# Performance work log

Hardware: AMD Instinct MI355X
Metric: run time of the kernel (lower is better)

## Reference

```python
import jax, jax.numpy as jnp
import numpy as np

NUM_HEADS = 16
HEAD_DIM = 128


def rotate_half(x):
    x1, x2 = jnp.split(x, 2, axis=-1)
    return jnp.concatenate((-x2, x1), axis=-1)


def setup_inputs() -> dict:
    key = jax.random.key(0)
    ks = jax.random.split(key, 6)
    B, S, H = 2, 2048, 2048
    hidden_states = jax.random.normal(ks[0], (B, S, H), dtype=jnp.float32)
    # RoPE cos/sin tables (HF-style: half-dim freqs duplicated)
    inv_freq = 1.0 / (10000.0 ** (jnp.arange(0, HEAD_DIM, 2, dtype=jnp.float32) / HEAD_DIM))
    t = jnp.arange(S, dtype=jnp.float32)
    freqs = jnp.outer(t, inv_freq)                      # [S, HEAD_DIM/2]
    emb = jnp.concatenate((freqs, freqs), axis=-1)      # [S, HEAD_DIM]
    cos = jnp.cos(emb)
    sin = jnp.sin(emb)
    attention_mask = jnp.zeros((1, 1, S, S), dtype=jnp.float32)
    scale = 0.02
    Wq = jax.random.normal(ks[1], (H, H), dtype=jnp.float32) * scale
    Wk = jax.random.normal(ks[2], (H, H), dtype=jnp.float32) * scale
    Wv = jax.random.normal(ks[3], (H, H), dtype=jnp.float32) * scale
    Wo = jax.random.normal(ks[4], (H, H), dtype=jnp.float32) * scale
    return {"hidden_states": hidden_states, "cos": cos, "sin": sin,
            "attention_mask": attention_mask, "Wq": Wq, "Wk": Wk, "Wv": Wv, "Wo": Wo}


def reference(hidden_states, cos, sin, attention_mask, Wq, Wk, Wv, Wo):
    B, S, H = hidden_states.shape
    nh, hd = NUM_HEADS, HEAD_DIM
    # nn.Linear(bias=False): x @ W.T
    q = hidden_states @ Wq.T
    k = hidden_states @ Wk.T
    v = hidden_states @ Wv.T
    # [B, nh, S, hd]
    q = q.reshape(B, S, nh, hd).transpose(0, 2, 1, 3)
    k = k.reshape(B, S, nh, hd).transpose(0, 2, 1, 3)
    v = v.reshape(B, S, nh, hd).transpose(0, 2, 1, 3)
    # RoPE
    c = cos[None, None, :, :]
    s = sin[None, None, :, :]
    q = q * c + rotate_half(q) * s
    k = k * c + rotate_half(k) * s
    scores = jnp.einsum("bhqd,bhkd->bhqk", q, k) / jnp.sqrt(jnp.float32(hd))
    scores = scores + attention_mask
    attn = jax.nn.softmax(scores, axis=-1)
    out = jnp.einsum("bhqk,bhkd->bhqd", attn, v)
    out = out.transpose(0, 2, 1, 3).reshape(B, S, H)
    return out @ Wo.T
```

## Files before the change

### kernel.cpp

```cpp
#include <hip/hip_runtime.h>
#include <stdint.h>

typedef __bf16 bf16;
typedef __attribute__((ext_vector_type(4))) __bf16 bf16x4;
typedef __attribute__((ext_vector_type(8))) __bf16 bf16x8;
typedef __attribute__((ext_vector_type(4))) float f32x4;
typedef __attribute__((ext_vector_type(4))) short short4v;

__device__ __forceinline__ void gl2lds16(const void* g, void* l) {
  __builtin_amdgcn_global_load_lds(
      (__attribute__((address_space(1))) void*)(uintptr_t)g,
      (__attribute__((address_space(3))) void*)(uint32_t)(uintptr_t)l,
      16, 0, 0);
}

__device__ __forceinline__ f32x4 mfma_16x16x16(bf16x4 a, bf16x4 b, f32x4 c) {
#if defined(__HIP_DEVICE_COMPILE__)
  return __builtin_amdgcn_mfma_f32_16x16x16bf16_1k(
      __builtin_bit_cast(short4v, a), __builtin_bit_cast(short4v, b), c, 0, 0, 0);
#else
  return c;
#endif
}

__global__ __launch_bounds__(256) void cast_to_bf16(const float* __restrict__ x,
                                                    bf16* __restrict__ y, int n4) {
  int i = blockIdx.x * 256 + threadIdx.x;
  if (i >= n4) return;
  float4 v = ((const float4*)x)[i];
  bf16x4 o;
  o[0] = (bf16)v.x; o[1] = (bf16)v.y; o[2] = (bf16)v.z; o[3] = (bf16)v.w;
  ((bf16x4*)y)[i] = o;
}

__global__ __launch_bounds__(256) void cast_w4(const float* __restrict__ s0,
                                               const float* __restrict__ s1,
                                               const float* __restrict__ s2,
                                               const float* __restrict__ s3,
                                               bf16* __restrict__ d0, bf16* __restrict__ d1,
                                               bf16* __restrict__ d2, bf16* __restrict__ d3) {
  int i = blockIdx.x * 256 + threadIdx.x;
  int wsel = i >> 20;
  int j = i & 1048575;
  const float* s = wsel == 0 ? s0 : wsel == 1 ? s1 : wsel == 2 ? s2 : s3;
  bf16* d = wsel == 0 ? d0 : wsel == 1 ? d1 : wsel == 2 ? d2 : d3;
  float4 v = ((const float4*)s)[j];
  bf16x4 o;
  o[0] = (bf16)v.x; o[1] = (bf16)v.y; o[2] = (bf16)v.z; o[3] = (bf16)v.w;
  ((bf16x4*)d)[j] = o;
}

template <typename OutT>
__global__ __launch_bounds__(512) void gemm256(const bf16* __restrict__ A,
                                               const bf16* __restrict__ B,
                                               OutT* __restrict__ C,
                                               int M, int N, int K) {
  __shared__ bf16 As[2][2][128 * 64];
  __shared__ bf16 Bs[2][2][128 * 64];
  const int t = threadIdx.x;
  const int w = t >> 6;
  const int lane = t & 63;
  const int quad = lane >> 4;
  const int m16 = lane & 15;
  const int wr = w >> 2;
  const int wc = w & 3;
  const size_t rowA0 = (size_t)blockIdx.y * 256;
  const size_t rowB0 = (size_t)blockIdx.x * 256;

  f32x4 acc[8][4];
#pragma unroll
  for (int i = 0; i < 8; ++i)
#pragma unroll
    for (int j = 0; j < 4; ++j) { f32x4 z = {0.f, 0.f, 0.f, 0.f}; acc[i][j] = z; }

  const int srow = lane >> 3;
  const int sg = (lane & 7) ^ (srow & 7);

  auto stage = [&](int buf, int kt) {
#pragma unroll
    for (int h = 0; h < 2; ++h)
#pragma unroll
      for (int i = 0; i < 2; ++i) {
        const int ch = w * 2 + i;
        const int r = h * 128 + ch * 8 + srow;
        gl2lds16(A + (rowA0 + r) * (size_t)K + kt * 64 + sg * 8, &As[buf][h][ch * 512]);
        gl2lds16(B + (rowB0 + r) * (size_t)K + kt * 64 + sg * 8, &Bs[buf][h][ch * 512]);
      }
  };

  stage(0, 0);
  asm volatile("s_waitcnt vmcnt(0)" ::: "memory");
  __builtin_amdgcn_s_barrier();

  const int NT = K >> 6;
#pragma unroll 1
  for (int kt = 0; kt < NT; ++kt) {
    const int c = kt & 1;
    if (kt + 1 < NT) stage(c ^ 1, kt + 1);

#pragma unroll
    for (int p = 0; p < 4; ++p) {
      const int mh = p >> 1;
      const int nh = p & 1;
      bf16x8 af[4][2], bfr[2][2];
#pragma unroll
      for (int fm = 0; fm < 4; ++fm)
#pragma unroll
        for (int ks = 0; ks < 2; ++ks) {
          const int r = (mh * 4 + fm) * 16 + m16;
          af[fm][ks] = *(const bf16x8*)&As[c][wr][r * 64 + (((ks * 4 + quad) ^ (m16 & 7)) * 8)];
        }
#pragma unroll
      for (int fn = 0; fn < 2; ++fn)
#pragma unroll
        for (int ks = 0; ks < 2; ++ks) {
          const int r = (wc & 1) * 64 + (nh * 2 + fn) * 16 + m16;
          bfr[fn][ks] = *(const bf16x8*)&Bs[c][wc >> 1][r * 64 + (((ks * 4 + quad) ^ (m16 & 7)) * 8)];
        }
      __builtin_amdgcn_s_setprio(1);
#pragma unroll
      for (int fm = 0; fm < 4; ++fm)
#pragma unroll
        for (int fn = 0; fn < 2; ++fn)
#pragma unroll
          for (int ks = 0; ks < 2; ++ks)
            acc[mh * 4 + fm][nh * 2 + fn] = __builtin_amdgcn_mfma_f32_16x16x32_bf16(
                af[fm][ks], bfr[fn][ks], acc[mh * 4 + fm][nh * 2 + fn], 0, 0, 0);
      __builtin_amdgcn_s_setprio(0);
      if (p < 3) __builtin_amdgcn_s_barrier();
    }
    asm volatile("s_waitcnt vmcnt(0)" ::: "memory");
    __builtin_amdgcn_s_barrier();
  }

#pragma unroll
  for (int fm = 0; fm < 8; ++fm)
#pragma unroll
    for (int fn = 0; fn < 4; ++fn)
#pragma unroll
      for (int r = 0; r < 4; ++r) {
        size_t row = rowA0 + wr * 128 + fm * 16 + quad * 4 + r;
        size_t col = rowB0 + wc * 64 + fn * 16 + m16;
        float v = acc[fm][fn][r];
        if constexpr (__is_same(OutT, float)) C[row * N + col] = v;
        else                                  C[row * N + col] = (bf16)v;
      }
}

__global__ __launch_bounds__(256) void rope_kernel(bf16* __restrict__ X,
                                                   const float* __restrict__ cosp,
                                                   const float* __restrict__ sinp) {
  int tid = blockIdx.x * 256 + threadIdx.x;
  int d = tid & 63;
  int hh = (tid >> 6) & 31;
  int tok = tid >> 11;
  if (tok >= 4096) return;
  int s = tok & 2047;
  const float sl2e = 0.088388347648318447f * 1.4426950408889634f;
  float qs = hh < 16 ? sl2e : 1.0f;
  size_t base = (size_t)tok * 4096 + hh * 128 + d;
  float c = cosp[s * 128 + d];
  float sn = sinp[s * 128 + d];
  float x1 = (float)X[base];
  float x2 = (float)X[base + 64];
  X[base]      = (bf16)((x1 * c - x2 * sn) * qs);
  X[base + 64] = (bf16)((x2 * c + x1 * sn) * qs);
}

__global__ __launch_bounds__(256) void flash_attn(const bf16* __restrict__ Qg,
                                                  const bf16* __restrict__ Kg,
                                                  const bf16* __restrict__ Vt,
                                                  bf16* __restrict__ O) {
  __shared__ bf16 Ks[2][64 * 128];
  __shared__ bf16 Vs[2][128 * 64];

  const int t = threadIdx.x;
  const int w = t >> 6;
  const int lane = t & 63;
  const int quad = lane >> 4;
  const int m16 = lane & 15;
  const int qt = blockIdx.x;
  const int bh = blockIdx.y;
  const int b = bh >> 4;
  const int h = bh & 15;

  bf16x8 qf[2][4];
#pragma unroll
  for (int half = 0; half < 2; ++half) {
    const int qrow = qt * 128 + w * 32 + half * 16 + m16;
    const bf16* qp = Qg + (size_t)(b * 2048 + qrow) * 4096 + h * 128 + quad * 8;
#pragma unroll
    for (int ks = 0; ks < 4; ++ks) qf[half][ks] = *(const bf16x8*)(qp + ks * 32);
  }

  const int krl = lane >> 4;
  const int vrl = lane >> 3;
  const int vg = (lane & 7) ^ (vrl & 7);

  auto stage = [&](int buf, int kt) {
#pragma unroll
    for (int i = 0; i < 4; ++i) {
      const int c = w * 4 + i;
      const int krow = c * 4 + krl;
      const int kgg = (lane & 15) ^ (krow & 15);
      gl2lds16(Kg + (size_t)(b * 2048 + kt * 64 + krow) * 4096 + h * 128 + kgg * 8,
               &Ks[buf][c * 512]);
      const int vrow = c * 8 + vrl;
      gl2lds16(Vt + (size_t)(h * 128 + vrow) * 4096 + b * 2048 + kt * 64 + vg * 8,
               &Vs[buf][c * 512]);
    }
  };

  f32x4 o[2][8];
#pragma unroll
  for (int half = 0; half < 2; ++half)
#pragma unroll
    for (int i = 0; i < 8; ++i) { f32x4 z = {0.f, 0.f, 0.f, 0.f}; o[half][i] = z; }
  float lsum[2] = {0.f, 0.f};

  stage(0, 0);

#pragma unroll 1
  for (int kt = 0; kt < 32; ++kt) {
    const int cur = kt & 1;
    __syncthreads();
    if (kt < 31) stage(cur ^ 1, kt + 1);

    f32x4 st[2][4];
#pragma unroll
    for (int half = 0; half < 2; ++half)
#pragma unroll
      for (int nb = 0; nb < 4; ++nb) {
        f32x4 z = {0.f, 0.f, 0.f, 0.f};
        st[half][nb] = z;
      }
    __builtin_amdgcn_s_setprio(1);
#pragma unroll
    for (int nb = 0; nb < 4; ++nb)
#pragma unroll
      for (int ks = 0; ks < 4; ++ks) {
        bf16x8 kf = *(const bf16x8*)&Ks[cur][(nb * 16 + m16) * 128 + ((ks * 4 + quad) ^ m16) * 8];
        st[0][nb] = __builtin_amdgcn_mfma_f32_16x16x32_bf16(kf, qf[0][ks], st[0][nb], 0, 0, 0);
        st[1][nb] = __builtin_amdgcn_mfma_f32_16x16x32_bf16(kf, qf[1][ks], st[1][nb], 0, 0, 0);
      }
    __builtin_amdgcn_s_setprio(0);

    bf16x4 pA[2][4];
#pragma unroll
    for (int half = 0; half < 2; ++half)
#pragma unroll
      for (int nb = 0; nb < 4; ++nb)
#pragma unroll
        for (int r = 0; r < 4; ++r) {
          float p = __builtin_amdgcn_exp2f(st[half][nb][r]);
          lsum[half] += p;
          pA[half][nb][r] = (bf16)p;
        }

    __builtin_amdgcn_s_setprio(1);
#pragma unroll
    for (int db = 0; db < 8; ++db)
#pragma unroll
      for (int nb = 0; nb < 4; ++nb) {
        bf16x4 vB = *(const bf16x4*)&Vs[cur][(db * 16 + m16) * 64 +
            (((nb * 2 + (quad >> 1)) ^ (m16 & 7)) * 8 + (quad & 1) * 4)];
        o[0][db] = mfma_16x16x16(vB, pA[0][nb], o[0][db]);
        o[1][db] = mfma_16x16x16(vB, pA[1][nb], o[1][db]);
      }
    __builtin_amdgcn_s_setprio(0);
  }

#pragma unroll
  for (int half = 0; half < 2; ++half) {
    lsum[half] += __shfl_xor(lsum[half], 16);
    lsum[half] += __shfl_xor(lsum[half], 32);
  }
  float inv[2] = {1.0f / lsum[0], 1.0f / lsum[1]};

#pragma unroll
  for (int half = 0; half < 2; ++half) {
    const int row = qt * 128 + w * 32 + half * 16 + m16;
    bf16* op = O + (size_t)(b * 2048 + row) * 2048 + h * 128 + quad * 4;
#pragma unroll
    for (int db = 0; db < 8; ++db) {
      bf16x4 ov;
#pragma unroll
      for (int r = 0; r < 4; ++r) ov[r] = (bf16)(o[half][db][r] * inv[half]);
      *(bf16x4*)(op + db * 16) = ov;
    }
  }
}

extern "C" void kernel_launch(void* const* d_in, const int* in_sizes, int n_in,
                              void* d_out, int out_size, void* d_ws, size_t ws_size,
                              hipStream_t stream) {
  const float* hs   = (const float*)d_in[0];
  const float* cosp = (const float*)d_in[1];
  const float* sinp = (const float*)d_in[2];
  const float* Wq   = (const float*)d_in[4];
  const float* Wk   = (const float*)d_in[5];
  const float* Wv   = (const float*)d_in[6];
  const float* Wo   = (const float*)d_in[7];
  float* out = (float*)d_out;

  char* ws = (char*)d_ws;
  bf16* Xb   = (bf16*)(ws);
  bf16* Wqkb = (bf16*)(ws + 16777216);
  bf16* Wvb  = (bf16*)(ws + 33554432);
  bf16* Wob  = (bf16*)(ws + 41943040);
  bf16* QKb  = (bf16*)(ws + 50331648);
  bf16* Vtb  = (bf16*)(ws + 83886080);
  bf16* Ob   = Xb;

  cast_to_bf16<<<8192, 256, 0, stream>>>(hs, Xb, 2097152);
  cast_w4<<<16384, 256, 0, stream>>>(Wq, Wk, Wv, Wo,
                                     Wqkb, Wqkb + 4194304, Wvb, Wob);

  gemm256<bf16><<<dim3(16, 16), 512, 0, stream>>>(Xb, Wqkb, QKb, 4096, 4096, 2048);
  gemm256<bf16><<<dim3(16, 8), 512, 0, stream>>>(Wvb, Xb, Vtb, 2048, 4096, 2048);

  rope_kernel<<<32768, 256, 0, stream>>>(QKb, cosp, sinp);

  flash_attn<<<dim3(16, 32), 256, 0, stream>>>(QKb, QKb + 2048, Vtb, Ob);

  gemm256<float><<<dim3(8, 16), 512, 0, stream>>>(Ob, Wob, out, 4096, 2048, 2048);
}
```

Before: 450.9 us.

## Template GEMM tile shapes and interleave prefetch loads across compute phases

Turns the fixed 256x256 GEMM into a template over block and warp-grid shape. The V-projection and output-projection GEMMs now use 128x256 and 256x128 tiles, which gives 256 blocks instead of 128 and fills more of the compute units. The next-tile global-to-LDS loads are also split across the MFMA phases instead of being issued all at once, so memory traffic overlaps with compute. The cost is smaller tiles with less data reuse for those two GEMMs, and a different barrier placement.

```diff
diff --git a/kernel.cpp b/kernel.cpp
--- a/kernel.cpp
+++ b/kernel.cpp
@@ -50,45 +50,54 @@
   ((bf16x4*)d)[j] = o;
 }
 
-template <typename OutT>
-__global__ __launch_bounds__(512) void gemm256(const bf16* __restrict__ A,
-                                               const bf16* __restrict__ B,
-                                               OutT* __restrict__ C,
-                                               int M, int N, int K) {
-  __shared__ bf16 As[2][2][128 * 64];
-  __shared__ bf16 Bs[2][2][128 * 64];
+template <int BM, int BN, int WGM, int WGN, typename OutT>
+__global__ __launch_bounds__(512) void gemm_t(const bf16* __restrict__ A,
+                                              const bf16* __restrict__ B,
+                                              OutT* __restrict__ C,
+                                              int M, int N, int K) {
+  constexpr int FM = BM / WGM / 16;
+  constexpr int FN = BN / WGN / 16;
+  constexpr int NPH = FM / 2;
+  constexpr int CH_A = BM / 8;
+  constexpr int CH_TOT = (BM + BN) / 8;
+  constexpr int CHW = CH_TOT / 8;
+
+  __shared__ bf16 As[2][BM * 64];
+  __shared__ bf16 Bs[2][BN * 64];
+
   const int t = threadIdx.x;
   const int w = t >> 6;
   const int lane = t & 63;
   const int quad = lane >> 4;
   const int m16 = lane & 15;
-  const int wr = w >> 2;
-  const int wc = w & 3;
-  const size_t rowA0 = (size_t)blockIdx.y * 256;
-  const size_t rowB0 = (size_t)blockIdx.x * 256;
-
-  f32x4 acc[8][4];
-#pragma unroll
-  for (int i = 0; i < 8; ++i)
-#pragma unroll
-    for (int j = 0; j < 4; ++j) { f32x4 z = {0.f, 0.f, 0.f, 0.f}; acc[i][j] = z; }
+  const int wr = w / WGN;
+  const int wc = w % WGN;
+  const size_t rowA0 = (size_t)blockIdx.y * BM;
+  const size_t rowB0 = (size_t)blockIdx.x * BN;
+
+  f32x4 acc[FM][FN];
+#pragma unroll
+  for (int i = 0; i < FM; ++i)
+#pragma unroll
+    for (int j = 0; j < FN; ++j) { f32x4 z = {0.f, 0.f, 0.f, 0.f}; acc[i][j] = z; }
 
   const int srow = lane >> 3;
   const int sg = (lane & 7) ^ (srow & 7);
 
-  auto stage = [&](int buf, int kt) {
-#pragma unroll
-    for (int h = 0; h < 2; ++h)
-#pragma unroll
-      for (int i = 0; i < 2; ++i) {
-        const int ch = w * 2 + i;
-        const int r = h * 128 + ch * 8 + srow;
-        gl2lds16(A + (rowA0 + r) * (size_t)K + kt * 64 + sg * 8, &As[buf][h][ch * 512]);
-        gl2lds16(B + (rowB0 + r) * (size_t)K + kt * 64 + sg * 8, &Bs[buf][h][ch * 512]);
-      }
+  auto stage1 = [&](int buf, int kt, int j) {
+    const int g = w * CHW + j;
+    if (g < CH_A) {
+      gl2lds16(A + (rowA0 + g * 8 + srow) * (size_t)K + kt * 64 + sg * 8,
+               &As[buf][g * 512]);
+    } else {
+      const int gb = g - CH_A;
+      gl2lds16(B + (rowB0 + gb * 8 + srow) * (size_t)K + kt * 64 + sg * 8,
+               &Bs[buf][gb * 512]);
+    }
   };
 
-  stage(0, 0);
+#pragma unroll
+  for (int j = 0; j < CHW; ++j) stage1(0, 0, j);
   asm volatile("s_waitcnt vmcnt(0)" ::: "memory");
   __builtin_amdgcn_s_barrier();
 
@@ -96,51 +105,56 @@
 #pragma unroll 1
   for (int kt = 0; kt < NT; ++kt) {
     const int c = kt & 1;
-    if (kt + 1 < NT) stage(c ^ 1, kt + 1);
-
-#pragma unroll
-    for (int p = 0; p < 4; ++p) {
-      const int mh = p >> 1;
-      const int nh = p & 1;
-      bf16x8 af[4][2], bfr[2][2];
-#pragma unroll
-      for (int fm = 0; fm < 4; ++fm)
-#pragma unroll
-        for (int ks = 0; ks < 2; ++ks) {
-          const int r = (mh * 4 + fm) * 16 + m16;
-          af[fm][ks] = *(const bf16x8*)&As[c][wr][r * 64 + (((ks * 4 + quad) ^ (m16 & 7)) * 8)];
-        }
-#pragma unroll
-      for (int fn = 0; fn < 2; ++fn)
-#pragma unroll
-        for (int ks = 0; ks < 2; ++ks) {
-          const int r = (wc & 1) * 64 + (nh * 2 + fn) * 16 + m16;
-          bfr[fn][ks] = *(const bf16x8*)&Bs[c][wc >> 1][r * 64 + (((ks * 4 + quad) ^ (m16 & 7)) * 8)];
-        }
+    const bool pf = (kt + 1 < NT);
+
+    bf16x8 bfr[FN][2];
+#pragma unroll
+    for (int p = 0; p < NPH; ++p) {
+      if (p == 0) {
+#pragma unroll
+        for (int fn = 0; fn < FN; ++fn)
+#pragma unroll
+          for (int ks = 0; ks < 2; ++ks)
+            bfr[fn][ks] = *(const bf16x8*)&Bs[c][((wc * FN + fn) * 16 + m16) * 64 +
+                                                 (((ks * 4 + quad) ^ (m16 & 7)) * 8)];
+      }
+      bf16x8 af[2][2];
+#pragma unroll
+      for (int mi = 0; mi < 2; ++mi)
+#pragma unroll
+        for (int ks = 0; ks < 2; ++ks)
+          af[mi][ks] = *(const bf16x8*)&As[c][((wr * FM + p * 2 + mi) * 16 + m16) * 64 +
+                                              (((ks * 4 + quad) ^ (m16 & 7)) * 8)];
+      if (pf) {
+#pragma unroll
+        for (int j = p * CHW / NPH; j < (p + 1) * CHW / NPH; ++j)
+          stage1(c ^ 1, kt + 1, j);
+      }
+      __builtin_amdgcn_s_barrier();
       __builtin_amdgcn_s_setprio(1);
 #pragma unroll
-      for (int fm = 0; fm < 4; ++fm)
-#pragma unroll
-        for (int fn = 0; fn < 2; ++fn)
+      for (int mi = 0; mi < 2; ++mi)
+#pragma unroll
+        for (int fn = 0; fn < FN; ++fn)
 #pragma unroll
           for (int ks = 0; ks < 2; ++ks)
-            acc[mh * 4 + fm][nh * 2 + fn] = __builtin_amdgcn_mfma_f32_16x16x32_bf16(
-                af[fm][ks], bfr[fn][ks], acc[mh * 4 + fm][nh * 2 + fn], 0, 0, 0);
+            acc[p * 2 + mi][fn] = __builtin_amdgcn_mfma_f32_16x16x32_bf16(
+                af[mi][ks], bfr[fn][ks], acc[p * 2 + mi][fn], 0, 0, 0);
       __builtin_amdgcn_s_setprio(0);
-      if (p < 3) __builtin_amdgcn_s_barrier();
+      if (p + 1 < NPH) __builtin_amdgcn_s_barrier();
     }
     asm volatile("s_waitcnt vmcnt(0)" ::: "memory");
     __builtin_amdgcn_s_barrier();
   }
 
 #pragma unroll
-  for (int fm = 0; fm < 8; ++fm)
-#pragma unroll
-    for (int fn = 0; fn < 4; ++fn)
+  for (int fm = 0; fm < FM; ++fm)
+#pragma unroll
+    for (int fn = 0; fn < FN; ++fn)
 #pragma unroll
       for (int r = 0; r < 4; ++r) {
-        size_t row = rowA0 + wr * 128 + fm * 16 + quad * 4 + r;
-        size_t col = rowB0 + wc * 64 + fn * 16 + m16;
+        size_t row = rowA0 + (wr * FM + fm) * 16 + quad * 4 + r;
+        size_t col = rowB0 + (wc * FN + fn) * 16 + m16;
         float v = acc[fm][fn][r];
         if constexpr (__is_same(OutT, float)) C[row * N + col] = v;
         else                                  C[row * N + col] = (bf16)v;
@@ -316,12 +330,15 @@
   cast_w4<<<16384, 256, 0, stream>>>(Wq, Wk, Wv, Wo,
                                      Wqkb, Wqkb + 4194304, Wvb, Wob);
 
-  gemm256<bf16><<<dim3(16, 16), 512, 0, stream>>>(Xb, Wqkb, QKb, 4096, 4096, 2048);
-  gemm256<bf16><<<dim3(16, 8), 512, 0, stream>>>(Wvb, Xb, Vtb, 2048, 4096, 2048);
+  gemm_t<256, 256, 2, 4, bf16><<<dim3(16, 16), 512, 0, stream>>>(
+      Xb, Wqkb, QKb, 4096, 4096, 2048);
+  gemm_t<128, 256, 2, 4, bf16><<<dim3(16, 16), 512, 0, stream>>>(
+      Wvb, Xb, Vtb, 2048, 4096, 2048);
 
   rope_kernel<<<32768, 256, 0, stream>>>(QKb, cosp, sinp);
 
   flash_attn<<<dim3(16, 32), 256, 0, stream>>>(QKb, QKb + 2048, Vtb, Ob);
 
-  gemm256<float><<<dim3(8, 16), 512, 0, stream>>>(Ob, Wob, out, 4096, 2048, 2048);
-}
+  gemm_t<256, 128, 4, 2, float><<<dim3(16, 16), 512, 0, stream>>>(
+      Ob, Wob, out, 4096, 2048, 2048);
+}
```

New measurement: 416.4 us. -7.6%, faster.
